# Performance work log

Hardware: AMD Instinct MI355X
Metric: run time of the kernel (lower is better)

The kernel has to match this reference:

```python
import jax, jax.numpy as jnp
import numpy as np

B, S, H = 2, 1024, 2048          # batch, seq, hidden_size
I = 7168                          # intermediate_size
E = 8                             # num_local_experts
TOPK = 2                          # num_experts_per_tok
R = int(I * H * 0.1 / (I + H))    # delta_low_rank = 159


def setup_inputs() -> dict:
    key = jax.random.key(0)
    ks = jax.random.split(key, 12)
    s = 0.02
    return {
        "hidden_states": jax.random.normal(ks[0], (B, S, H), jnp.float32),
        "gate_w": jax.random.normal(ks[1], (E, H), jnp.float32) * s,
        "W1": jax.random.normal(ks[2], (E, I, H), jnp.float32) * s,
        "W2": jax.random.normal(ks[3], (E, H, I), jnp.float32) * s,
        "W3": jax.random.normal(ks[4], (E, I, H), jnp.float32) * s,
        "U1": jax.random.normal(ks[5], (E, I, R), jnp.float32) * s,
        "V1": jax.random.normal(ks[6], (E, R, H), jnp.float32) * s,
        "U2": jax.random.normal(ks[7], (E, H, R), jnp.float32) * s,
        "V2": jax.random.normal(ks[8], (E, R, I), jnp.float32) * s,
        "U3": jax.random.normal(ks[9], (E, I, R), jnp.float32) * s,
        "V3": jax.random.normal(ks[10], (E, R, H), jnp.float32) * s,
    }


def reference(hidden_states, gate_w, W1, W2, W3, U1, V1, U2, V2, U3, V3):
    b, s, h = hidden_states.shape
    x = hidden_states.reshape(-1, h)                     # [T, H]
    T = x.shape[0]
    router_logits = x @ gate_w.T                          # [T, E]
    probs = jax.nn.softmax(router_logits.astype(jnp.float32), axis=-1)
    rw, sel = jax.lax.top_k(probs, TOPK)                  # [T, k]
    rw = rw / jnp.sum(rw, axis=-1, keepdims=True)
    rw = rw.astype(x.dtype)
    # dense combine weights: zero for unselected experts (same math as gather/scatter)
    comb = jnp.zeros((T, E), x.dtype).at[jnp.arange(T)[:, None], sel].add(rw)
    out = jnp.zeros_like(x)
    for e in range(E):                                    # small fixed expert loop
        up = x @ W3[e].T + (x @ V3[e].T) @ U3[e].T        # [T, I]
        gate = x @ W1[e].T + (x @ V1[e].T) @ U1[e].T      # [T, I]
        hmid = jax.nn.silu(gate) * up                     # [T, I]
        y = hmid @ W2[e].T + (hmid @ V2[e].T) @ U2[e].T   # [T, H]
        out = out + comb[:, e, None] * y
    return out.reshape(b, s, h), router_logits
```

## Files before the change

### kernel.cpp

```cpp
#include <hip/hip_runtime.h>
#include <cstdint>
#include <cstddef>

#define TT 2048
#define HH 2048
#define II 7168
#define EE 8
#define RR 159
#define RPAD 192
#define ROWS 4096

typedef __attribute__((ext_vector_type(8))) short bf16x8;
typedef __attribute__((ext_vector_type(4))) float f32x4;

__device__ __forceinline__ unsigned short f2bf(float f) {
  unsigned int u = __float_as_uint(f);
  u += 0x7fffu + ((u >> 16) & 1u);
  return (unsigned short)(u >> 16);
}
__device__ __forceinline__ float bf2f(unsigned short u) {
  return __uint_as_float(((unsigned int)u) << 16);
}
__device__ __forceinline__ unsigned int cvtpk(float lo, float hi) {
  unsigned int r;
  asm volatile("v_cvt_pk_bf16_f32 %0, %1, %2" : "=v"(r) : "v"(lo), "v"(hi));
  return r;
}
__device__ __forceinline__ bf16x8 zero8() {
  bf16x8 v;
#pragma unroll
  for (int j = 0; j < 8; j++) v[j] = 0;
  return v;
}
__device__ __forceinline__ void gload16(const unsigned short* g, unsigned short* l) {
  __builtin_amdgcn_global_load_lds(
      (const __attribute__((address_space(1))) unsigned int*)g,
      (__attribute__((address_space(3))) unsigned int*)l, 16, 0, 0);
}

__global__ __launch_bounds__(256) void k_f2bf_flat(const float* __restrict__ s,
                                                   unsigned short* __restrict__ d,
                                                   long long n8) {
  long long i = (long long)blockIdx.x * blockDim.x + threadIdx.x;
  long long stride = (long long)gridDim.x * blockDim.x;
  for (; i < n8; i += stride) {
    const float* p = s + i * 8;
    float4 a = *(const float4*)p;
    float4 b = *(const float4*)(p + 4);
    bf16x8 v;
    v[0] = (short)f2bf(a.x); v[1] = (short)f2bf(a.y);
    v[2] = (short)f2bf(a.z); v[3] = (short)f2bf(a.w);
    v[4] = (short)f2bf(b.x); v[5] = (short)f2bf(b.y);
    v[6] = (short)f2bf(b.z); v[7] = (short)f2bf(b.w);
    *(bf16x8*)(d + i * 8) = v;
  }
}

__global__ __launch_bounds__(256) void k_upad(const float* __restrict__ U,
                                              unsigned short* __restrict__ Up, int rows) {
  long long idx = (long long)blockIdx.x * 256 + threadIdx.x;
  long long total = (long long)rows * 24;
  if (idx >= total) return;
  int row = (int)(idx / 24), c8 = (int)(idx % 24);
  unsigned short* dp = Up + (size_t)row * RPAD + c8 * 8;
#pragma unroll
  for (int j = 0; j < 8; j++) {
    int c = c8 * 8 + j;
    dp[j] = (c < RR) ? f2bf(U[(size_t)row * RR + c]) : (unsigned short)0;
  }
}

__global__ __launch_bounds__(256) void k_router(
    const float* __restrict__ x, const float* __restrict__ gw,
    float* __restrict__ logits_out, int* __restrict__ sel,
    float* __restrict__ wtok, int* __restrict__ counts) {
  int t = blockIdx.x;
  const float* xr = x + (size_t)t * HH;
  int base = threadIdx.x * 8;
  float4 x0 = *(const float4*)(xr + base);
  float4 x1 = *(const float4*)(xr + base + 4);
  float part[EE];
#pragma unroll
  for (int e = 0; e < EE; e++) {
    const float* g = gw + (size_t)e * HH + base;
    float4 g0 = *(const float4*)g;
    float4 g1 = *(const float4*)(g + 4);
    part[e] = x0.x * g0.x + x0.y * g0.y + x0.z * g0.z + x0.w * g0.w +
              x1.x * g1.x + x1.y * g1.y + x1.z * g1.z + x1.w * g1.w;
  }
#pragma unroll
  for (int off = 32; off > 0; off >>= 1)
#pragma unroll
    for (int e = 0; e < EE; e++) part[e] += __shfl_down(part[e], off);
  __shared__ float red[4][EE];
  int w = threadIdx.x >> 6, lane = threadIdx.x & 63;
  if (lane == 0) {
#pragma unroll
    for (int e = 0; e < EE; e++) red[w][e] = part[e];
  }
  __syncthreads();
  if (threadIdx.x == 0) {
    float lg[EE];
    float mx = -1e30f;
#pragma unroll
    for (int e = 0; e < EE; e++) {
      lg[e] = red[0][e] + red[1][e] + red[2][e] + red[3][e];
      logits_out[(size_t)t * EE + e] = lg[e];
      mx = fmaxf(mx, lg[e]);
    }
    float p[EE];
#pragma unroll
    for (int e = 0; e < EE; e++) p[e] = __expf(lg[e] - mx);
    int i0 = 0;
#pragma unroll
    for (int e = 1; e < EE; e++)
      if (lg[e] > lg[i0]) i0 = e;
    int i1 = (i0 == 0) ? 1 : 0;
#pragma unroll
    for (int e = 0; e < EE; e++)
      if (e != i0 && lg[e] > lg[i1]) i1 = e;
    float s = p[i0] + p[i1];
    sel[t * 2] = i0;
    sel[t * 2 + 1] = i1;
    wtok[t * 2] = p[i0] / s;
    wtok[t * 2 + 1] = p[i1] / s;
    atomicAdd(&counts[i0], 1);
    atomicAdd(&counts[i1], 1);
  }
}

__global__ void k_offsets(const int* __restrict__ counts, int* __restrict__ offs,
                          int* __restrict__ curs) {
  if (threadIdx.x == 0 && blockIdx.x == 0) {
    int o = 0;
    for (int e = 0; e < EE; e++) {
      offs[e] = o;
      curs[e] = o;
      o += counts[e];
    }
    offs[EE] = o;
  }
}

__global__ void k_build(const int* __restrict__ sel, const float* __restrict__ wtok,
                        int* __restrict__ curs, int* __restrict__ rowsA,
                        float* __restrict__ rowwgt, int* __restrict__ rowid) {
  int t = blockIdx.x * blockDim.x + threadIdx.x;
  if (t >= TT) return;
  for (int k = 0; k < 2; k++) {
    int e = sel[t * 2 + k];
    int pos = atomicAdd(&curs[e], 1);
    rowsA[pos] = t;
    rowwgt[pos] = wtok[t * 2 + k];
    rowid[t * 2 + k] = pos;
  }
}

__global__ void k_x2bf(const float* __restrict__ x, unsigned short* __restrict__ xb) {
  size_t i = (size_t)blockIdx.x * blockDim.x + threadIdx.x;
  size_t n8 = (size_t)TT * HH / 8;
  size_t stride = (size_t)gridDim.x * blockDim.x;
  for (size_t idx = i; idx < n8; idx += stride) {
    const float* s = x + idx * 8;
    float4 a = *(const float4*)s;
    float4 b = *(const float4*)(s + 4);
    bf16x8 v;
    v[0] = (short)f2bf(a.x); v[1] = (short)f2bf(a.y);
    v[2] = (short)f2bf(a.z); v[3] = (short)f2bf(a.w);
    v[4] = (short)f2bf(b.x); v[5] = (short)f2bf(b.y);
    v[6] = (short)f2bf(b.z); v[7] = (short)f2bf(b.w);
    *(bf16x8*)(xb + idx * 8) = v;
  }
}

template <bool GATHER>
__global__ __launch_bounds__(256, 2) void k_lowrank_sk(
    const unsigned short* __restrict__ Ab, int lda, int K, int kc, int NS,
    const unsigned short* __restrict__ V0, const unsigned short* __restrict__ V1,
    float* __restrict__ Pp,
    const int* __restrict__ counts, const int* __restrict__ offs,
    const int* __restrict__ rowsA) {
  int e = blockIdx.y;
  int cnt = counts[e];
  int m0 = blockIdx.x * 64;
  if (m0 >= cnt) return;
  int roff = offs[e];
  int mat = blockIdx.z / NS, split = blockIdx.z % NS;
  const unsigned short* V = ((mat == 0) ? V0 : V1) + (size_t)e * RR * K;
  float* Pout = Pp + (size_t)blockIdx.z * ROWS * RPAD;
  int kt0 = split * kc;
  int kt1 = kt0 + kc;
  if (kt1 > K) kt1 = K;
  __shared__ unsigned short As[64 * 64];
  __shared__ unsigned short Bs[192 * 64];
  int tid = threadIdx.x, lane = tid & 63, w = tid >> 6;
  int rstage = tid >> 3, cg = tid & 7;
  f32x4 acc[12];
#pragma unroll
  for (int n = 0; n < 12; n++) acc[n] = (f32x4){0.f, 0.f, 0.f, 0.f};
  for (int kt = kt0; kt < kt1; kt += 64) {
#pragma unroll
    for (int p = 0; p < 2; p++) {
      int r = p * 32 + rstage;
      bf16x8 v = zero8();
      int gr = m0 + r;
      if (gr < cnt) {
        size_t arow = GATHER ? (size_t)rowsA[roff + gr] : (size_t)(roff + gr);
        v = *(const bf16x8*)(Ab + arow * (size_t)lda + kt + cg * 8);
      }
      *(bf16x8*)&As[r * 64 + ((cg ^ (r & 7)) * 8)] = v;
    }
#pragma unroll
    for (int p = 0; p < 6; p++) {
      int r = p * 32 + rstage;
      bf16x8 v = zero8();
      if (r < RR) v = *(const bf16x8*)(V + (size_t)r * K + kt + cg * 8);
      *(bf16x8*)&Bs[r * 64 + ((cg ^ (r & 7)) * 8)] = v;
    }
    __syncthreads();
#pragma unroll
    for (int ks = 0; ks < 2; ks++) {
      int rA = w * 16 + (lane & 15);
      bf16x8 a = *(const bf16x8*)&As[rA * 64 + (((ks * 4 + (lane >> 4)) ^ (rA & 7)) * 8)];
#pragma unroll
      for (int n = 0; n < 12; n++) {
        int rB = n * 16 + (lane & 15);
        bf16x8 b = *(const bf16x8*)&Bs[rB * 64 + (((ks * 4 + (lane >> 4)) ^ (rB & 7)) * 8)];
        acc[n] = __builtin_amdgcn_mfma_f32_16x16x32_bf16(a, b, acc[n], 0, 0, 0);
      }
    }
    __syncthreads();
  }
  int mbase = m0 + w * 16 + (lane >> 4) * 4;
#pragma unroll
  for (int n = 0; n < 12; n++) {
    int col = n * 16 + (lane & 15);
#pragma unroll
    for (int r4 = 0; r4 < 4; r4++) {
      int row = mbase + r4;
      if (row < cnt) Pout[(size_t)(roff + row) * RPAD + col] = acc[n][r4];
    }
  }
}

__global__ __launch_bounds__(256) void k_lr_reduce(
    const float* __restrict__ Pp, unsigned short* __restrict__ P0,
    unsigned short* __restrict__ P1m, int NS, int nmat) {
  long long idx = (long long)blockIdx.x * 256 + threadIdx.x;
  long long total = (long long)nmat * ROWS * 24;
  if (idx >= total) return;
  int mat = (int)(idx / ((long long)ROWS * 24));
  int rem = (int)(idx % ((long long)ROWS * 24));
  int row = rem / 24, c8 = rem % 24;
  const float* base = Pp + ((size_t)mat * NS) * ROWS * RPAD + (size_t)row * RPAD + c8 * 8;
  float s0 = 0, s1 = 0, s2 = 0, s3 = 0, s4 = 0, s5 = 0, s6 = 0, s7 = 0;
  for (int sp = 0; sp < NS; sp++) {
    const float* p = base + (size_t)sp * ROWS * RPAD;
    float4 a = *(const float4*)p;
    float4 b = *(const float4*)(p + 4);
    s0 += a.x; s1 += a.y; s2 += a.z; s3 += a.w;
    s4 += b.x; s5 += b.y; s6 += b.z; s7 += b.w;
  }
  bf16x8 v;
  v[0] = (short)f2bf(s0); v[1] = (short)f2bf(s1);
  v[2] = (short)f2bf(s2); v[3] = (short)f2bf(s3);
  v[4] = (short)f2bf(s4); v[5] = (short)f2bf(s5);
  v[6] = (short)f2bf(s6); v[7] = (short)f2bf(s7);
  unsigned short* P = (mat == 0) ? P0 : P1m;
  *(bf16x8*)(P + (size_t)row * RPAD + c8 * 8) = v;
}

template <int MODE>
__global__ __launch_bounds__(256, 2) void k_gemm(
    const unsigned short* __restrict__ Ab, int K, int N,
    const float* __restrict__ Wf,
    const unsigned short* __restrict__ Pq,
    const unsigned short* __restrict__ Uq,
    const unsigned short* __restrict__ Gb,
    const float* __restrict__ rowwgt,
    unsigned short* __restrict__ outb,
    float* __restrict__ outf,
    const int* __restrict__ counts, const int* __restrict__ offs,
    const int* __restrict__ rowsA) {
  int e = blockIdx.z;
  int cnt = counts[e];
  int m0 = blockIdx.y * 128;
  if (m0 >= cnt) return;
  int n0 = blockIdx.x * 128;
  int roff = offs[e];
  const float* w = Wf + (size_t)e * (size_t)N * K;
  const unsigned short* uq = Uq + (size_t)e * (size_t)N * RPAD;
  __shared__ unsigned short As[128 * 64];
  __shared__ unsigned short Bs[128 * 64];
  int tid = threadIdx.x, lane = tid & 63, wv = tid >> 6;
  int wr = (wv >> 1) * 64, wc = (wv & 1) * 64;
  f32x4 acc[4][4];
#pragma unroll
  for (int m = 0; m < 4; m++)
#pragma unroll
    for (int n = 0; n < 4; n++) acc[m][n] = (f32x4){0.f, 0.f, 0.f, 0.f};
  int srow = (wv << 5) + (lane >> 3);
  int swz = (((lane & 7) ^ ((lane >> 3) & 7)) << 3);
  const unsigned short* pa[4];
  const float* pw[4];
#pragma unroll
  for (int i = 0; i < 4; i++) {
    int gr = m0 + srow + i * 8;
    if (gr >= cnt) gr = cnt - 1;
    size_t arow = (MODE < 2) ? (size_t)rowsA[roff + gr] : (size_t)(roff + gr);
    pa[i] = Ab + arow * (size_t)K + swz;
    pw[i] = w + (size_t)(n0 + srow + i * 8) * K + swz;
  }
  float4 rb[4][2];
#pragma unroll
  for (int i = 0; i < 4; i++) {
    rb[i][0] = *(const float4*)(pw[i]);
    rb[i][1] = *(const float4*)(pw[i] + 4);
  }
  for (int kt = 0; kt < K; kt += 64) {
#pragma unroll
    for (int i = 0; i < 4; i++) {
      gload16(pa[i] + kt, &As[((wv << 5) + (i << 3)) * 64]);
      int idx = (srow + i * 8) * 64 + (lane & 7) * 8;
      uint4 q;
      q.x = cvtpk(rb[i][0].x, rb[i][0].y);
      q.y = cvtpk(rb[i][0].z, rb[i][0].w);
      q.z = cvtpk(rb[i][1].x, rb[i][1].y);
      q.w = cvtpk(rb[i][1].z, rb[i][1].w);
      *(uint4*)&Bs[idx] = q;
    }
    __syncthreads();
    if (kt + 64 < K) {
#pragma unroll
      for (int i = 0; i < 4; i++) {
        rb[i][0] = *(const float4*)(pw[i] + kt + 64);
        rb[i][1] = *(const float4*)(pw[i] + kt + 68);
      }
    }
#pragma unroll
    for (int ks = 0; ks < 2; ks++) {
      bf16x8 af[4], bs[4];
#pragma unroll
      for (int m = 0; m < 4; m++) {
        int r = wr + m * 16 + (lane & 15);
        af[m] = *(const bf16x8*)&As[r * 64 + (((ks * 4 + (lane >> 4)) ^ (r & 7)) * 8)];
      }
#pragma unroll
      for (int n = 0; n < 4; n++) {
        int r = wc + n * 16 + (lane & 15);
        bs[n] = *(const bf16x8*)&Bs[r * 64 + (((ks * 4 + (lane >> 4)) ^ (r & 7)) * 8)];
      }
#pragma unroll
      for (int m = 0; m < 4; m++)
#pragma unroll
        for (int n = 0; n < 4; n++)
          acc[m][n] = __builtin_amdgcn_mfma_f32_16x16x32_bf16(af[m], bs[n], acc[m][n], 0, 0, 0);
    }
    __syncthreads();
  }
  for (int kt = 0; kt < RPAD; kt += 64) {
#pragma unroll
    for (int i = 0; i < 4; i++) {
      int gr = m0 + srow + i * 8;
      if (gr >= cnt) gr = cnt - 1;
      gload16(Pq + (size_t)(roff + gr) * RPAD + swz + kt, &As[((wv << 5) + (i << 3)) * 64]);
      gload16(uq + (size_t)(n0 + srow + i * 8) * RPAD + swz + kt,
              &Bs[((wv << 5) + (i << 3)) * 64]);
    }
    __syncthreads();
#pragma unroll
    for (int ks = 0; ks < 2; ks++) {
      bf16x8 af[4], bs[4];
#pragma unroll
      for (int m = 0; m < 4; m++) {
        int r = wr + m * 16 + (lane & 15);
        af[m] = *(const bf16x8*)&As[r * 64 + (((ks * 4 + (lane >> 4)) ^ (r & 7)) * 8)];
      }
#pragma unroll
      for (int n = 0; n < 4; n++) {
        int r = wc + n * 16 + (lane & 15);
        bs[n] = *(const bf16x8*)&Bs[r * 64 + (((ks * 4 + (lane >> 4)) ^ (r & 7)) * 8)];
      }
#pragma unroll
      for (int m = 0; m < 4; m++)
#pragma unroll
        for (int n = 0; n < 4; n++)
          acc[m][n] = __builtin_amdgcn_mfma_f32_16x16x32_bf16(af[m], bs[n], acc[m][n], 0, 0, 0);
    }
    __syncthreads();
  }
#pragma unroll
  for (int m = 0; m < 4; m++) {
#pragma unroll
    for (int r4 = 0; r4 < 4; r4++) {
      int row = m0 + wr + m * 16 + (lane >> 4) * 4 + r4;
      if (row < cnt) {
        size_t rbase = (size_t)(roff + row) * N + n0 + wc;
        if constexpr (MODE == 0) {
#pragma unroll
          for (int n = 0; n < 4; n++)
            outb[rbase + n * 16 + (lane & 15)] = f2bf(acc[m][n][r4]);
        } else if constexpr (MODE == 1) {
#pragma unroll
          for (int n = 0; n < 4; n++) {
            float g = bf2f(Gb[rbase + n * 16 + (lane & 15)]);
            float uu = acc[m][n][r4];
            float h = (g / (1.f + __expf(-g))) * uu;
            outb[rbase + n * 16 + (lane & 15)] = f2bf(h);
          }
        } else {
          float wgt = rowwgt[roff + row];
#pragma unroll
          for (int n = 0; n < 4; n++)
            outf[rbase + n * 16 + (lane & 15)] = acc[m][n][r4] * wgt;
        }
      }
    }
  }
}

__global__ void k_combine(const float* __restrict__ ybuf, const int* __restrict__ rowid,
                          float* __restrict__ out) {
  int idx = blockIdx.x * 256 + threadIdx.x;
  int t = idx >> 8;
  int c = (idx & 255) * 8;
  int r0 = rowid[t * 2], r1 = rowid[t * 2 + 1];
  const float* y0 = ybuf + (size_t)r0 * HH + c;
  const float* y1 = ybuf + (size_t)r1 * HH + c;
  float4 a0 = *(const float4*)y0, a1 = *(const float4*)(y0 + 4);
  float4 b0 = *(const float4*)y1, b1 = *(const float4*)(y1 + 4);
  float4 o0 = {a0.x + b0.x, a0.y + b0.y, a0.z + b0.z, a0.w + b0.w};
  float4 o1 = {a1.x + b1.x, a1.y + b1.y, a1.z + b1.z, a1.w + b1.w};
  float* o = out + (size_t)t * HH + c;
  *(float4*)o = o0;
  *(float4*)(o + 4) = o1;
}

extern "C" void kernel_launch(void* const* d_in, const int* in_sizes, int n_in,
                              void* d_out, int out_size, void* d_ws, size_t ws_size,
                              hipStream_t stream) {
  const float* x  = (const float*)d_in[0];
  const float* gw = (const float*)d_in[1];
  const float* W1 = (const float*)d_in[2];
  const float* W2 = (const float*)d_in[3];
  const float* W3 = (const float*)d_in[4];
  const float* U1 = (const float*)d_in[5];
  const float* V1 = (const float*)d_in[6];
  const float* U2 = (const float*)d_in[7];
  const float* V2 = (const float*)d_in[8];
  const float* U3 = (const float*)d_in[9];
  const float* V3 = (const float*)d_in[10];
  float* out = (float*)d_out;
  float* logits = out + (size_t)TT * HH;

  char* ws = (char*)d_ws;
  size_t off = 0;
  auto take = [&](size_t b) -> char* {
    char* p = ws + off;
    off += (b + 255) & ~(size_t)255;
    return p;
  };
  unsigned short* Xb   = (unsigned short*)take((size_t)TT * HH * 2);
  unsigned short* hmid = (unsigned short*)take((size_t)ROWS * II * 2);
  unsigned short* Gbuf = (unsigned short*)take((size_t)ROWS * II * 2);
  unsigned short* P1   = (unsigned short*)take((size_t)ROWS * RPAD * 2);
  unsigned short* P3   = (unsigned short*)take((size_t)ROWS * RPAD * 2);
  unsigned short* P2   = (unsigned short*)take((size_t)ROWS * RPAD * 2);
  float* ybuf          = (float*)take((size_t)ROWS * HH * 4);
  int* sel             = (int*)take((size_t)TT * 2 * 4);
  float* wtok          = (float*)take((size_t)TT * 2 * 4);
  int* rowsA           = (int*)take((size_t)ROWS * 4);
  float* rowwgt        = (float*)take((size_t)ROWS * 4);
  int* rowid           = (int*)take((size_t)TT * 2 * 4);
  int* meta            = (int*)take(1024);
  int* counts  = meta;
  int* offs    = meta + 16;
  int* curs    = meta + 32;
  unsigned short* V1b = (unsigned short*)take((size_t)EE * RR * HH * 2);
  unsigned short* V3b = (unsigned short*)take((size_t)EE * RR * HH * 2);
  unsigned short* V2b = (unsigned short*)take((size_t)EE * RR * II * 2);
  unsigned short* U1p = (unsigned short*)take((size_t)EE * II * RPAD * 2);
  unsigned short* U3p = (unsigned short*)take((size_t)EE * II * RPAD * 2);
  unsigned short* U2p = (unsigned short*)take((size_t)EE * HH * RPAD * 2);
  float* Pp           = (float*)take((size_t)8 * ROWS * RPAD * 4);

  hipMemsetAsync(counts, 0, EE * sizeof(int), stream);
  k_f2bf_flat<<<1024, 256, 0, stream>>>(V1, V1b, (long long)EE * RR * HH / 8);
  k_f2bf_flat<<<1024, 256, 0, stream>>>(V3, V3b, (long long)EE * RR * HH / 8);
  k_f2bf_flat<<<1024, 256, 0, stream>>>(V2, V2b, (long long)EE * RR * II / 8);
  k_upad<<<(EE * II * 24 + 255) / 256, 256, 0, stream>>>(U1, U1p, EE * II);
  k_upad<<<(EE * II * 24 + 255) / 256, 256, 0, stream>>>(U3, U3p, EE * II);
  k_upad<<<(EE * HH * 24 + 255) / 256, 256, 0, stream>>>(U2, U2p, EE * HH);
  k_router<<<TT, 256, 0, stream>>>(x, gw, logits, sel, wtok, counts);
  k_offsets<<<1, 64, 0, stream>>>(counts, offs, curs);
  k_build<<<TT / 256, 256, 0, stream>>>(sel, wtok, curs, rowsA, rowwgt, rowid);
  k_x2bf<<<2048, 256, 0, stream>>>(x, Xb);
  k_lowrank_sk<true><<<dim3(TT / 64, EE, 2 * 4), 256, 0, stream>>>(
      Xb, HH, HH, 512, 4, V1b, V3b, Pp, counts, offs, rowsA);
  k_lr_reduce<<<(2 * ROWS * 24 + 255) / 256, 256, 0, stream>>>(Pp, P1, P3, 4, 2);
  k_gemm<0><<<dim3(II / 128, TT / 128, EE), 256, 0, stream>>>(
      Xb, HH, II, W1, P1, U1p, nullptr, nullptr, Gbuf, nullptr, counts, offs, rowsA);
  k_gemm<1><<<dim3(II / 128, TT / 128, EE), 256, 0, stream>>>(
      Xb, HH, II, W3, P3, U3p, Gbuf, nullptr, hmid, nullptr, counts, offs, rowsA);
  k_lowrank_sk<false><<<dim3(TT / 64, EE, 8), 256, 0, stream>>>(
      hmid, II, II, 896, 8, V2b, V2b, Pp, counts, offs, rowsA);
  k_lr_reduce<<<(ROWS * 24 + 255) / 256, 256, 0, stream>>>(Pp, P2, P2, 8, 1);
  k_gemm<2><<<dim3(HH / 128, TT / 128, EE), 256, 0, stream>>>(
      hmid, II, HH, W2, P2, U2p, nullptr, rowwgt, nullptr, ybuf, counts, offs, rowsA);
  k_combine<<<(TT * HH / 8) / 256, 256, 0, stream>>>(ybuf, rowid, out);
}
```

Measured before the change: 1.200 ms.

## Use 256x128 tiles for gate/up expert GEMMs and split down-proj kernel

```diff
diff --git a/kernel.cpp b/kernel.cpp
--- a/kernel.cpp
+++ b/kernel.cpp
@@ -271,17 +271,160 @@
 }
 
 template <int MODE>
-__global__ __launch_bounds__(256, 2) void k_gemm(
+__global__ __launch_bounds__(256, 2) void k_gemm_big(
     const unsigned short* __restrict__ Ab, int K, int N,
     const float* __restrict__ Wf,
     const unsigned short* __restrict__ Pq,
     const unsigned short* __restrict__ Uq,
     const unsigned short* __restrict__ Gb,
-    const float* __restrict__ rowwgt,
     unsigned short* __restrict__ outb,
-    float* __restrict__ outf,
     const int* __restrict__ counts, const int* __restrict__ offs,
     const int* __restrict__ rowsA) {
+  int e = blockIdx.z;
+  int cnt = counts[e];
+  int m0 = blockIdx.y * 256;
+  if (m0 >= cnt) return;
+  int n0 = blockIdx.x * 128;
+  int roff = offs[e];
+  const float* w = Wf + (size_t)e * (size_t)N * K;
+  const unsigned short* uq = Uq + (size_t)e * (size_t)N * RPAD;
+  __shared__ unsigned short As[256 * 64];
+  __shared__ unsigned short Bs[128 * 64];
+  int tid = threadIdx.x, lane = tid & 63, wv = tid >> 6;
+  f32x4 acc[4][8];
+#pragma unroll
+  for (int m = 0; m < 4; m++)
+#pragma unroll
+    for (int n = 0; n < 8; n++) acc[m][n] = (f32x4){0.f, 0.f, 0.f, 0.f};
+  int swz = (((lane & 7) ^ ((lane >> 3) & 7)) << 3);
+  int srowA = (wv << 6) + (lane >> 3);
+  int aoff[8];
+#pragma unroll
+  for (int i = 0; i < 8; i++) {
+    int gr = m0 + srowA + i * 8;
+    if (gr >= cnt) gr = cnt - 1;
+    int arow = (MODE < 2) ? rowsA[roff + gr] : (roff + gr);
+    aoff[i] = arow * K + swz;
+  }
+  int srowB = (wv << 5) + (lane >> 3);
+  int woff[4];
+#pragma unroll
+  for (int i = 0; i < 4; i++) woff[i] = (n0 + srowB + i * 8) * K + swz;
+  float4 rb[4][2];
+#pragma unroll
+  for (int i = 0; i < 4; i++) {
+    rb[i][0] = *(const float4*)(w + woff[i]);
+    rb[i][1] = *(const float4*)(w + woff[i] + 4);
+  }
+  for (int kt = 0; kt < K; kt += 64) {
+#pragma unroll
+    for (int i = 0; i < 8; i++)
+      gload16(Ab + aoff[i] + kt, &As[((wv << 6) + (i << 3)) * 64]);
+#pragma unroll
+    for (int i = 0; i < 4; i++) {
+      int idx = (srowB + i * 8) * 64 + (lane & 7) * 8;
+      uint4 q;
+      q.x = cvtpk(rb[i][0].x, rb[i][0].y);
+      q.y = cvtpk(rb[i][0].z, rb[i][0].w);
+      q.z = cvtpk(rb[i][1].x, rb[i][1].y);
+      q.w = cvtpk(rb[i][1].z, rb[i][1].w);
+      *(uint4*)&Bs[idx] = q;
+    }
+    __syncthreads();
+    if (kt + 64 < K) {
+#pragma unroll
+      for (int i = 0; i < 4; i++) {
+        rb[i][0] = *(const float4*)(w + woff[i] + kt + 64);
+        rb[i][1] = *(const float4*)(w + woff[i] + kt + 68);
+      }
+    }
+#pragma unroll
+    for (int ks = 0; ks < 2; ks++) {
+      bf16x8 af[4], bs[8];
+#pragma unroll
+      for (int m = 0; m < 4; m++) {
+        int r = (wv << 6) + m * 16 + (lane & 15);
+        af[m] = *(const bf16x8*)&As[r * 64 + (((ks * 4 + (lane >> 4)) ^ (r & 7)) * 8)];
+      }
+#pragma unroll
+      for (int n = 0; n < 8; n++) {
+        int r = n * 16 + (lane & 15);
+        bs[n] = *(const bf16x8*)&Bs[r * 64 + (((ks * 4 + (lane >> 4)) ^ (r & 7)) * 8)];
+      }
+#pragma unroll
+      for (int m = 0; m < 4; m++)
+#pragma unroll
+        for (int n = 0; n < 8; n++)
+          acc[m][n] = __builtin_amdgcn_mfma_f32_16x16x32_bf16(af[m], bs[n], acc[m][n], 0, 0, 0);
+    }
+    __syncthreads();
+  }
+  for (int kt = 0; kt < RPAD; kt += 64) {
+#pragma unroll
+    for (int i = 0; i < 8; i++) {
+      int gr = m0 + srowA + i * 8;
+      if (gr >= cnt) gr = cnt - 1;
+      gload16(Pq + (size_t)(roff + gr) * RPAD + swz + kt, &As[((wv << 6) + (i << 3)) * 64]);
+    }
+#pragma unroll
+    for (int i = 0; i < 4; i++)
+      gload16(uq + (size_t)(n0 + srowB + i * 8) * RPAD + swz + kt,
+              &Bs[((wv << 5) + (i << 3)) * 64]);
+    __syncthreads();
+#pragma unroll
+    for (int ks = 0; ks < 2; ks++) {
+      bf16x8 af[4], bs[8];
+#pragma unroll
+      for (int m = 0; m < 4; m++) {
+        int r = (wv << 6) + m * 16 + (lane & 15);
+        af[m] = *(const bf16x8*)&As[r * 64 + (((ks * 4 + (lane >> 4)) ^ (r & 7)) * 8)];
+      }
+#pragma unroll
+      for (int n = 0; n < 8; n++) {
+        int r = n * 16 + (lane & 15);
+        bs[n] = *(const bf16x8*)&Bs[r * 64 + (((ks * 4 + (lane >> 4)) ^ (r & 7)) * 8)];
+      }
+#pragma unroll
+      for (int m = 0; m < 4; m++)
+#pragma unroll
+        for (int n = 0; n < 8; n++)
+          acc[m][n] = __builtin_amdgcn_mfma_f32_16x16x32_bf16(af[m], bs[n], acc[m][n], 0, 0, 0);
+    }
+    __syncthreads();
+  }
+#pragma unroll
+  for (int m = 0; m < 4; m++) {
+#pragma unroll
+    for (int r4 = 0; r4 < 4; r4++) {
+      int row = m0 + (wv << 6) + m * 16 + (lane >> 4) * 4 + r4;
+      if (row < cnt) {
+        size_t rbase = (size_t)(roff + row) * N + n0;
+        if constexpr (MODE == 0) {
+#pragma unroll
+          for (int n = 0; n < 8; n++)
+            outb[rbase + n * 16 + (lane & 15)] = f2bf(acc[m][n][r4]);
+        } else {
+#pragma unroll
+          for (int n = 0; n < 8; n++) {
+            float g = bf2f(Gb[rbase + n * 16 + (lane & 15)]);
+            float uu = acc[m][n][r4];
+            float h = (g / (1.f + __expf(-g))) * uu;
+            outb[rbase + n * 16 + (lane & 15)] = f2bf(h);
+          }
+        }
+      }
+    }
+  }
+}
+
+__global__ __launch_bounds__(256, 2) void k_gemm_down(
+    const unsigned short* __restrict__ Ab, int K, int N,
+    const float* __restrict__ Wf,
+    const unsigned short* __restrict__ Pq,
+    const unsigned short* __restrict__ Uq,
+    const float* __restrict__ rowwgt,
+    float* __restrict__ outf,
+    const int* __restrict__ counts, const int* __restrict__ offs) {
   int e = blockIdx.z;
   int cnt = counts[e];
   int m0 = blockIdx.y * 128;
@@ -301,26 +444,24 @@
     for (int n = 0; n < 4; n++) acc[m][n] = (f32x4){0.f, 0.f, 0.f, 0.f};
   int srow = (wv << 5) + (lane >> 3);
   int swz = (((lane & 7) ^ ((lane >> 3) & 7)) << 3);
-  const unsigned short* pa[4];
-  const float* pw[4];
+  int aoff[4], woff[4];
 #pragma unroll
   for (int i = 0; i < 4; i++) {
     int gr = m0 + srow + i * 8;
     if (gr >= cnt) gr = cnt - 1;
-    size_t arow = (MODE < 2) ? (size_t)rowsA[roff + gr] : (size_t)(roff + gr);
-    pa[i] = Ab + arow * (size_t)K + swz;
-    pw[i] = w + (size_t)(n0 + srow + i * 8) * K + swz;
+    aoff[i] = (roff + gr) * K + swz;
+    woff[i] = (n0 + srow + i * 8) * K + swz;
   }
   float4 rb[4][2];
 #pragma unroll
   for (int i = 0; i < 4; i++) {
-    rb[i][0] = *(const float4*)(pw[i]);
-    rb[i][1] = *(const float4*)(pw[i] + 4);
+    rb[i][0] = *(const float4*)(w + woff[i]);
+    rb[i][1] = *(const float4*)(w + woff[i] + 4);
   }
   for (int kt = 0; kt < K; kt += 64) {
 #pragma unroll
     for (int i = 0; i < 4; i++) {
-      gload16(pa[i] + kt, &As[((wv << 5) + (i << 3)) * 64]);
+      gload16(Ab + aoff[i] + kt, &As[((wv << 5) + (i << 3)) * 64]);
       int idx = (srow + i * 8) * 64 + (lane & 7) * 8;
       uint4 q;
       q.x = cvtpk(rb[i][0].x, rb[i][0].y);
@@ -333,8 +474,8 @@
     if (kt + 64 < K) {
 #pragma unroll
       for (int i = 0; i < 4; i++) {
-        rb[i][0] = *(const float4*)(pw[i] + kt + 64);
-        rb[i][1] = *(const float4*)(pw[i] + kt + 68);
+        rb[i][0] = *(const float4*)(w + woff[i] + kt + 64);
+        rb[i][1] = *(const float4*)(w + woff[i] + kt + 68);
       }
     }
 #pragma unroll
@@ -395,25 +536,11 @@
     for (int r4 = 0; r4 < 4; r4++) {
       int row = m0 + wr + m * 16 + (lane >> 4) * 4 + r4;
       if (row < cnt) {
+        float wgt = rowwgt[roff + row];
         size_t rbase = (size_t)(roff + row) * N + n0 + wc;
-        if constexpr (MODE == 0) {
-#pragma unroll
-          for (int n = 0; n < 4; n++)
-            outb[rbase + n * 16 + (lane & 15)] = f2bf(acc[m][n][r4]);
-        } else if constexpr (MODE == 1) {
-#pragma unroll
-          for (int n = 0; n < 4; n++) {
-            float g = bf2f(Gb[rbase + n * 16 + (lane & 15)]);
-            float uu = acc[m][n][r4];
-            float h = (g / (1.f + __expf(-g))) * uu;
-            outb[rbase + n * 16 + (lane & 15)] = f2bf(h);
-          }
-        } else {
-          float wgt = rowwgt[roff + row];
-#pragma unroll
-          for (int n = 0; n < 4; n++)
-            outf[rbase + n * 16 + (lane & 15)] = acc[m][n][r4] * wgt;
-        }
+#pragma unroll
+        for (int n = 0; n < 4; n++)
+          outf[rbase + n * 16 + (lane & 15)] = acc[m][n][r4] * wgt;
       }
     }
   }
@@ -498,14 +625,14 @@
   k_lowrank_sk<true><<<dim3(TT / 64, EE, 2 * 4), 256, 0, stream>>>(
       Xb, HH, HH, 512, 4, V1b, V3b, Pp, counts, offs, rowsA);
   k_lr_reduce<<<(2 * ROWS * 24 + 255) / 256, 256, 0, stream>>>(Pp, P1, P3, 4, 2);
-  k_gemm<0><<<dim3(II / 128, TT / 128, EE), 256, 0, stream>>>(
-      Xb, HH, II, W1, P1, U1p, nullptr, nullptr, Gbuf, nullptr, counts, offs, rowsA);
-  k_gemm<1><<<dim3(II / 128, TT / 128, EE), 256, 0, stream>>>(
-      Xb, HH, II, W3, P3, U3p, Gbuf, nullptr, hmid, nullptr, counts, offs, rowsA);
+  k_gemm_big<0><<<dim3(II / 128, ROWS / 256, EE), 256, 0, stream>>>(
+      Xb, HH, II, W1, P1, U1p, nullptr, Gbuf, counts, offs, rowsA);
+  k_gemm_big<1><<<dim3(II / 128, ROWS / 256, EE), 256, 0, stream>>>(
+      Xb, HH, II, W3, P3, U3p, Gbuf, hmid, counts, offs, rowsA);
   k_lowrank_sk<false><<<dim3(TT / 64, EE, 8), 256, 0, stream>>>(
       hmid, II, II, 896, 8, V2b, V2b, Pp, counts, offs, rowsA);
   k_lr_reduce<<<(ROWS * 24 + 255) / 256, 256, 0, stream>>>(Pp, P2, P2, 8, 1);
-  k_gemm<2><<<dim3(HH / 128, TT / 128, EE), 256, 0, stream>>>(
-      hmid, II, HH, W2, P2, U2p, nullptr, rowwgt, nullptr, ybuf, counts, offs, rowsA);
+  k_gemm_down<<<dim3(HH / 128, TT / 128, EE), 256, 0, stream>>>(
+      hmid, II, HH, W2, P2, U2p, rowwgt, ybuf, counts, offs);
   k_combine<<<(TT * HH / 8) / 256, 256, 0, stream>>>(ybuf, rowid, out);
 }
```

After: 1.177 ms. Within noise of the previous version (-1.9%).

## Double-buffer LDS tiles in expert GEMM to overlap loads with MFMA

Applied to the files above, without the earlier changes.

```diff
diff --git a/kernel.cpp b/kernel.cpp
--- a/kernel.cpp
+++ b/kernel.cpp
@@ -271,7 +271,7 @@
 }
 
 template <int MODE>
-__global__ __launch_bounds__(256, 2) void k_gemm(
+__global__ __launch_bounds__(256, 2) void k_gemm2(
     const unsigned short* __restrict__ Ab, int K, int N,
     const float* __restrict__ Wf,
     const unsigned short* __restrict__ Pq,
@@ -290,8 +290,8 @@
   int roff = offs[e];
   const float* w = Wf + (size_t)e * (size_t)N * K;
   const unsigned short* uq = Uq + (size_t)e * (size_t)N * RPAD;
-  __shared__ unsigned short As[128 * 64];
-  __shared__ unsigned short Bs[128 * 64];
+  __shared__ unsigned short As[2][128 * 64];
+  __shared__ unsigned short Bs[2][128 * 64];
   int tid = threadIdx.x, lane = tid & 63, wv = tid >> 6;
   int wr = (wv >> 1) * 64, wc = (wv & 1) * 64;
   f32x4 acc[4][4];
@@ -301,60 +301,75 @@
     for (int n = 0; n < 4; n++) acc[m][n] = (f32x4){0.f, 0.f, 0.f, 0.f};
   int srow = (wv << 5) + (lane >> 3);
   int swz = (((lane & 7) ^ ((lane >> 3) & 7)) << 3);
-  const unsigned short* pa[4];
-  const float* pw[4];
+  int aoff[4], woff[4];
 #pragma unroll
   for (int i = 0; i < 4; i++) {
     int gr = m0 + srow + i * 8;
     if (gr >= cnt) gr = cnt - 1;
-    size_t arow = (MODE < 2) ? (size_t)rowsA[roff + gr] : (size_t)(roff + gr);
-    pa[i] = Ab + arow * (size_t)K + swz;
-    pw[i] = w + (size_t)(n0 + srow + i * 8) * K + swz;
+    int arow = (MODE < 2) ? rowsA[roff + gr] : (roff + gr);
+    aoff[i] = arow * K + swz;
+    woff[i] = (n0 + srow + i * 8) * K + swz;
   }
   float4 rb[4][2];
 #pragma unroll
   for (int i = 0; i < 4; i++) {
-    rb[i][0] = *(const float4*)(pw[i]);
-    rb[i][1] = *(const float4*)(pw[i] + 4);
-  }
-  for (int kt = 0; kt < K; kt += 64) {
-#pragma unroll
-    for (int i = 0; i < 4; i++) {
-      gload16(pa[i] + kt, &As[((wv << 5) + (i << 3)) * 64]);
-      int idx = (srow + i * 8) * 64 + (lane & 7) * 8;
-      uint4 q;
-      q.x = cvtpk(rb[i][0].x, rb[i][0].y);
-      q.y = cvtpk(rb[i][0].z, rb[i][0].w);
-      q.z = cvtpk(rb[i][1].x, rb[i][1].y);
-      q.w = cvtpk(rb[i][1].z, rb[i][1].w);
-      *(uint4*)&Bs[idx] = q;
-    }
-    __syncthreads();
-    if (kt + 64 < K) {
+    gload16(Ab + aoff[i], &As[0][((wv << 5) + (i << 3)) * 64]);
+    rb[i][0] = *(const float4*)(w + woff[i]);
+    rb[i][1] = *(const float4*)(w + woff[i] + 4);
+  }
+#pragma unroll
+  for (int i = 0; i < 4; i++) {
+    int idx = (srow + i * 8) * 64 + (lane & 7) * 8;
+    uint4 q;
+    q.x = cvtpk(rb[i][0].x, rb[i][0].y);
+    q.y = cvtpk(rb[i][0].z, rb[i][0].w);
+    q.z = cvtpk(rb[i][1].x, rb[i][1].y);
+    q.w = cvtpk(rb[i][1].z, rb[i][1].w);
+    *(uint4*)&Bs[0][idx] = q;
+  }
+  __syncthreads();
+  int nt = K >> 6;
+  for (int t = 0; t < nt; ++t) {
+    int cur = t & 1, nxt = cur ^ 1;
+    bool more = (t + 1 < nt);
+    if (more) {
 #pragma unroll
       for (int i = 0; i < 4; i++) {
-        rb[i][0] = *(const float4*)(pw[i] + kt + 64);
-        rb[i][1] = *(const float4*)(pw[i] + kt + 68);
+        gload16(Ab + aoff[i] + (t + 1) * 64, &As[nxt][((wv << 5) + (i << 3)) * 64]);
+        rb[i][0] = *(const float4*)(w + woff[i] + (t + 1) * 64);
+        rb[i][1] = *(const float4*)(w + woff[i] + (t + 1) * 64 + 4);
       }
     }
 #pragma unroll
     for (int ks = 0; ks < 2; ks++) {
-      bf16x8 af[4], bs[4];
+      bf16x8 af[4], bsr[4];
 #pragma unroll
       for (int m = 0; m < 4; m++) {
         int r = wr + m * 16 + (lane & 15);
-        af[m] = *(const bf16x8*)&As[r * 64 + (((ks * 4 + (lane >> 4)) ^ (r & 7)) * 8)];
+        af[m] = *(const bf16x8*)&As[cur][r * 64 + (((ks * 4 + (lane >> 4)) ^ (r & 7)) * 8)];
       }
 #pragma unroll
       for (int n = 0; n < 4; n++) {
         int r = wc + n * 16 + (lane & 15);
-        bs[n] = *(const bf16x8*)&Bs[r * 64 + (((ks * 4 + (lane >> 4)) ^ (r & 7)) * 8)];
+        bsr[n] = *(const bf16x8*)&Bs[cur][r * 64 + (((ks * 4 + (lane >> 4)) ^ (r & 7)) * 8)];
       }
 #pragma unroll
       for (int m = 0; m < 4; m++)
 #pragma unroll
         for (int n = 0; n < 4; n++)
-          acc[m][n] = __builtin_amdgcn_mfma_f32_16x16x32_bf16(af[m], bs[n], acc[m][n], 0, 0, 0);
+          acc[m][n] = __builtin_amdgcn_mfma_f32_16x16x32_bf16(af[m], bsr[n], acc[m][n], 0, 0, 0);
+    }
+    if (more) {
+#pragma unroll
+      for (int i = 0; i < 4; i++) {
+        int idx = (srow + i * 8) * 64 + (lane & 7) * 8;
+        uint4 q;
+        q.x = cvtpk(rb[i][0].x, rb[i][0].y);
+        q.y = cvtpk(rb[i][0].z, rb[i][0].w);
+        q.z = cvtpk(rb[i][1].x, rb[i][1].y);
+        q.w = cvtpk(rb[i][1].z, rb[i][1].w);
+        *(uint4*)&Bs[nxt][idx] = q;
+      }
     }
     __syncthreads();
   }
@@ -363,29 +378,29 @@
     for (int i = 0; i < 4; i++) {
       int gr = m0 + srow + i * 8;
       if (gr >= cnt) gr = cnt - 1;
-      gload16(Pq + (size_t)(roff + gr) * RPAD + swz + kt, &As[((wv << 5) + (i << 3)) * 64]);
+      gload16(Pq + (size_t)(roff + gr) * RPAD + swz + kt, &As[0][((wv << 5) + (i << 3)) * 64]);
       gload16(uq + (size_t)(n0 + srow + i * 8) * RPAD + swz + kt,
-              &Bs[((wv << 5) + (i << 3)) * 64]);
+              &Bs[0][((wv << 5) + (i << 3)) * 64]);
     }
     __syncthreads();
 #pragma unroll
     for (int ks = 0; ks < 2; ks++) {
-      bf16x8 af[4], bs[4];
+      bf16x8 af[4], bsr[4];
 #pragma unroll
       for (int m = 0; m < 4; m++) {
         int r = wr + m * 16 + (lane & 15);
-        af[m] = *(const bf16x8*)&As[r * 64 + (((ks * 4 + (lane >> 4)) ^ (r & 7)) * 8)];
+        af[m] = *(const bf16x8*)&As[0][r * 64 + (((ks * 4 + (lane >> 4)) ^ (r & 7)) * 8)];
       }
 #pragma unroll
       for (int n = 0; n < 4; n++) {
         int r = wc + n * 16 + (lane & 15);
-        bs[n] = *(const bf16x8*)&Bs[r * 64 + (((ks * 4 + (lane >> 4)) ^ (r & 7)) * 8)];
+        bsr[n] = *(const bf16x8*)&Bs[0][r * 64 + (((ks * 4 + (lane >> 4)) ^ (r & 7)) * 8)];
       }
 #pragma unroll
       for (int m = 0; m < 4; m++)
 #pragma unroll
         for (int n = 0; n < 4; n++)
-          acc[m][n] = __builtin_amdgcn_mfma_f32_16x16x32_bf16(af[m], bs[n], acc[m][n], 0, 0, 0);
+          acc[m][n] = __builtin_amdgcn_mfma_f32_16x16x32_bf16(af[m], bsr[n], acc[m][n], 0, 0, 0);
     }
     __syncthreads();
   }
@@ -498,14 +513,14 @@
   k_lowrank_sk<true><<<dim3(TT / 64, EE, 2 * 4), 256, 0, stream>>>(
       Xb, HH, HH, 512, 4, V1b, V3b, Pp, counts, offs, rowsA);
   k_lr_reduce<<<(2 * ROWS * 24 + 255) / 256, 256, 0, stream>>>(Pp, P1, P3, 4, 2);
-  k_gemm<0><<<dim3(II / 128, TT / 128, EE), 256, 0, stream>>>(
+  k_gemm2<0><<<dim3(II / 128, TT / 128, EE), 256, 0, stream>>>(
       Xb, HH, II, W1, P1, U1p, nullptr, nullptr, Gbuf, nullptr, counts, offs, rowsA);
-  k_gemm<1><<<dim3(II / 128, TT / 128, EE), 256, 0, stream>>>(
+  k_gemm2<1><<<dim3(II / 128, TT / 128, EE), 256, 0, stream>>>(
       Xb, HH, II, W3, P3, U3p, Gbuf, nullptr, hmid, nullptr, counts, offs, rowsA);
   k_lowrank_sk<false><<<dim3(TT / 64, EE, 8), 256, 0, stream>>>(
       hmid, II, II, 896, 8, V2b, V2b, Pp, counts, offs, rowsA);
   k_lr_reduce<<<(ROWS * 24 + 255) / 256, 256, 0, stream>>>(Pp, P2, P2, 8, 1);
-  k_gemm<2><<<dim3(HH / 128, TT / 128, EE), 256, 0, stream>>>(
+  k_gemm2<2><<<dim3(HH / 128, TT / 128, EE), 256, 0, stream>>>(
       hmid, II, HH, W2, P2, U2p, nullptr, rowwgt, nullptr, ybuf, counts, offs, rowsA);
   k_combine<<<(TT * HH / 8) / 256, 256, 0, stream>>>(ybuf, rowid, out);
 }
```

Measured after the change: 1.378 ms. +14.8%, slower.
